# Kernel optimization log

Hardware: AMD Instinct MI355X
Metric: run time of the kernel (lower is better)

## Reference

```python
import jax, jax.numpy as jnp
import numpy as np

N_QUBITS = 21
N_LAYERS = 3

# standard CNOT (control = first wire), reshaped for tensor contraction
_CNOT = np.array([[1, 0, 0, 0],
                  [0, 1, 0, 0],
                  [0, 0, 0, 1],
                  [0, 0, 1, 0]], dtype=np.complex64).reshape(2, 2, 2, 2)


def _rot(phi, theta, omega):
    """Rot(phi, theta, omega) = RZ(omega) RY(theta) RZ(phi), 2x2 complex64."""
    c = jnp.cos(theta * 0.5)
    s = jnp.sin(theta * 0.5)
    ep = jnp.exp(-0.5j * (phi + omega))   # e^{-i(phi+omega)/2}
    em = jnp.exp(0.5j * (phi - omega))    # e^{+i(phi-omega)/2}
    row0 = jnp.stack([ep * c, -em * s])
    row1 = jnp.stack([jnp.conj(em) * s, jnp.conj(ep) * c])
    return jnp.stack([row0, row1])


def _apply_1q(U, state, q):
    # contract gate with qubit axis q of state (shape (2,)*n)
    return jnp.moveaxis(jnp.tensordot(U, state, axes=((1,), (q,))), 0, q)


def _apply_cnot(state, q):
    # CNOT on adjacent qubits (q, q+1)
    out = jnp.tensordot(jnp.asarray(_CNOT), state, axes=((2, 3), (q, q + 1)))
    return jnp.moveaxis(out, (0, 1), (q, q + 1))


def _classifier(param, feat):
    n_layers, n_qubits = param.shape[0], param.shape[1]
    state = feat.astype(jnp.complex64).reshape((2,) * n_qubits)
    for i in range(n_layers):
        # layer of single-qubit Rot gates (== kron of per-qubit 2x2 unitaries)
        for j in range(n_qubits):
            U = _rot(param[i, j, 0], param[i, j, 1], param[i, j, 2])
            state = _apply_1q(U, state, j)
        # CNOT_layer: first pairs (0,1),(2,3),... then pairs (1,2),(3,4),...
        for q in range(0, n_qubits - 1, 2):
            state = _apply_cnot(state, q)
        for q in range(1, n_qubits - 1, 2):
            state = _apply_cnot(state, q)
    # sum over even flat indices == last qubit in |0>
    amp0 = state[..., 0]
    return jnp.sum(amp0.real ** 2 + amp0.imag ** 2)


def setup_inputs() -> dict:
    key = jax.random.key(0)
    k1, k2 = jax.random.split(key)
    feat = jax.random.normal(k1, (2 ** N_QUBITS,), dtype=jnp.float32)
    param = jax.random.uniform(k2, (N_LAYERS, N_QUBITS, 3),
                               dtype=jnp.float32,
                               minval=0.0, maxval=2.0 * np.pi)
    return {"feat": feat, "param": param}


def reference(feat, param):
    return _classifier(param, feat)
```

## Files before the change

### kernel.cpp

```cpp
#include <hip/hip_runtime.h>
#include <hip/hip_fp16.h>


typedef __attribute__((ext_vector_type(2))) float f2;

union H4 { int4 i4; __half2 h[4]; };
union H2 { int2 i2; __half2 h[2]; };

__device__ __forceinline__ f2 mkf2(float a, float b) { f2 r; r.x = a; r.y = b; return r; }

__device__ __forceinline__ unsigned SWZ(unsigned i) {
    return i ^ ((i >> 4) & 0xFu) ^ ((i >> 8) & 0xFu);
}
__device__ __forceinline__ unsigned f1(unsigned x, unsigned m) {
    return x ^ ((x >> 1) & m);
}
__device__ __forceinline__ unsigned f2fold(unsigned x, unsigned mA, unsigned mB) {
    unsigned t = x ^ ((x >> 1) & mA);
    return t ^ ((t >> 1) & mB);
}

__device__ __forceinline__ void crot(const f2 u00, const f2 u01,
                                     const f2 u10, const f2 u11,
                                     f2& a, f2& b) {
    const f2 sa = mkf2(-a.y, a.x);
    const f2 sb = mkf2(-b.y, b.x);
    f2 na = u00.x * a;
    na += u00.y * sa;
    na += u01.x * b;
    na += u01.y * sb;
    f2 nb = u10.x * a;
    nb += u10.y * sa;
    nb += u11.x * b;
    nb += u11.y * sb;
    a = na; b = nb;
}

__device__ __forceinline__ void apply4(f2 v[16], const f2* gU,
                                       int id0, int id1, int id2, int id3) {
    const int ids[4] = {id0, id1, id2, id3};
#pragma unroll
    for (int kk = 0; kk < 4; ++kk) {
        const int id = ids[kk];
        if (id < 0) continue;
        const f2 u00 = gU[4*id+0], u01 = gU[4*id+1];
        const f2 u10 = gU[4*id+2], u11 = gU[4*id+3];
#pragma unroll
        for (int x = 0; x < 16; ++x)
            if (!(x & (1 << kk)))
                crot(u00, u01, u10, u11, v[x], v[x | (1 << kk)]);
    }
}

__device__ __forceinline__ void prep_gates_lds(const float* __restrict__ param,
                                               f2* gU, unsigned tid) {
    if (tid < 63) {
        float phi = param[3*tid+0], th = param[3*tid+1], om = param[3*tid+2];
        float s, c;   __sincosf(0.5f*th, &s, &c);
        float sp, cp; __sincosf(-0.5f*(phi+om), &sp, &cp);
        float sm, cm; __sincosf( 0.5f*(phi-om), &sm, &cm);
        gU[4*tid+0] = mkf2( cp*c,  sp*c);
        gU[4*tid+1] = mkf2(-cm*s, -sm*s);
        gU[4*tid+2] = mkf2( cm*s, -sm*s);
        gU[4*tid+3] = mkf2( cp*c, -sp*c);
    }
}

__device__ __forceinline__ unsigned E1A (unsigned t, unsigned r){ return (t<<4)|r; }
__device__ __forceinline__ unsigned E2A (unsigned t, unsigned r){ return ((t>>4)<<8)|(r<<4)|(t&15u); }
__device__ __forceinline__ unsigned E3A (unsigned t, unsigned r){ return ((t>>8)<<12)|(r<<8)|(t&255u); }
__device__ __forceinline__ unsigned E4A (unsigned t, unsigned r){
    return (t&127u) | (((t>>7)&3u)<<10) | ((r&1u)<<7) | (((r>>1)&1u)<<8) | (((r>>2)&1u)<<9) | (((r>>3)&1u)<<12);
}
__device__ __forceinline__ unsigned E5A (unsigned t, unsigned r){
    return (t&31u) | (((t>>5)&7u)<<7) | (((t>>8)&1u)<<12) | ((r&1u)<<5) | (((r>>1)&1u)<<6) | (((r>>2)&1u)<<10) | (((r>>3)&1u)<<11);
}
__device__ __forceinline__ unsigned E6A (unsigned t, unsigned r){ return (t&1u) | (((t>>1)&255u)<<5) | (r<<1); }
__device__ __forceinline__ unsigned E7A (unsigned t, unsigned r){
    return ((t&63u)<<1) | (((t>>6)&7u)<<10) | (r&1u) | (((r>>1)&1u)<<7) | (((r>>2)&1u)<<8) | (((r>>3)&1u)<<9);
}
__device__ __forceinline__ unsigned E8A (unsigned t, unsigned r){ return (t&7u) | (((t>>3)&63u)<<7) | ((r&15u)<<3); }
__device__ __forceinline__ unsigned E11A(unsigned t, unsigned r){
    return (r&7u) | (((r>>3)&1u)<<8) | ((t&15u)<<9) | ((t>>4)<<3);
}
__device__ __forceinline__ unsigned E1Bn(unsigned t, unsigned r){ return (t&127u) | (r<<7); }
__device__ __forceinline__ unsigned E2Bn(unsigned t, unsigned r){ return (t&7u) | (r<<3) | ((t>>3)<<7); }
__device__ __forceinline__ unsigned E5Bn(unsigned t, unsigned r){
    return (t&3u) | ((r&1u)<<2) | (((t>>2)&31u)<<3) | (((r>>1)&1u)<<8) | (((r>>2)&1u)<<9) | (((r>>3)&1u)<<10);
}
__device__ __forceinline__ unsigned E6Bn(unsigned t, unsigned r){ return (t&15u) | (r<<4) | ((t>>4)<<8); }
__device__ __forceinline__ unsigned E7Bn(unsigned t, unsigned r){ return (r&15u) | (t<<4); }

template<class FW, class FR>
__device__ __forceinline__ void phase16(f2* buf, f2 v[16], unsigned tid, FW fw, FR fr) {
    const unsigned wb = fw(tid, 0u);
#pragma unroll
    for (unsigned r = 0; r < 16; ++r) buf[wb ^ fw(0u, r)] = v[r];
    __syncthreads();
    const unsigned rb = fr(tid, 0u);
#pragma unroll
    for (unsigned r = 0; r < 16; ++r) v[r] = buf[rb ^ fr(0u, r)];
}
template<class FW, class FR>
__device__ __forceinline__ void phase16_nb(f2* buf, f2 v[16], unsigned tid, FW fw, FR fr) {
    const unsigned wb = fw(tid, 0u);
#pragma unroll
    for (unsigned r = 0; r < 16; ++r) buf[wb ^ fw(0u, r)] = v[r];
    const unsigned rb = fr(tid, 0u);
#pragma unroll
    for (unsigned r = 0; r < 16; ++r) v[r] = buf[rb ^ fr(0u, r)];
}

__global__ __launch_bounds__(512, 2) void sweepA(const float* __restrict__ feat,
                                                 const float* __restrict__ param,
                                                 __half2* __restrict__ zbuf,
                                                 float* __restrict__ out) {
    __shared__ f2 sh0[8192];
    __shared__ f2 sh1[8192];
    __shared__ f2 gU[252];
    const unsigned tid = threadIdx.x;
    const unsigned F = blockIdx.x;
    if (F == 0 && tid == 0) out[0] = 0.0f;

    float4 fraw[4];
    {
        const float4* fp = (const float4*)(feat + (((size_t)F) << 13) + (tid << 4));
#pragma unroll
        for (int c = 0; c < 4; ++c) fraw[c] = fp[c];
    }
    prep_gates_lds(param, gU, tid);

    f2 v[16];
#pragma unroll
    for (int c = 0; c < 4; ++c) {
        v[4*c+0] = mkf2(fraw[c].x, 0.f); v[4*c+1] = mkf2(fraw[c].y, 0.f);
        v[4*c+2] = mkf2(fraw[c].z, 0.f); v[4*c+3] = mkf2(fraw[c].w, 0.f);
    }
    __syncthreads();

    apply4(v, gU, 20, 19, 18, 17);
    phase16_nb(sh0, v, tid,
        [](unsigned t, unsigned r){ return SWZ(E1A(t,r)); },
        [](unsigned t, unsigned r){ return SWZ(E2A(t,r)); });
    apply4(v, gU, 16, 15, 14, 13);
    phase16(sh1, v, tid,
        [](unsigned t, unsigned r){ return SWZ(E2A(t,r)); },
        [](unsigned t, unsigned r){ return SWZ(E3A(t,r)); });
    apply4(v, gU, 12, 11, 10, 9);
    phase16(sh0, v, tid,
        [](unsigned t, unsigned r){ return SWZ(E3A(t,r)); },
        [](unsigned t, unsigned r){ return SWZ(f2fold(E4A(t,r), 0x155u, 0x2AAu)); });
    apply4(v, gU, 34, 33, 32, 8);
    phase16(sh1, v, tid,
        [](unsigned t, unsigned r){ return SWZ(E4A(t,r)); },
        [](unsigned t, unsigned r){ return SWZ(f2fold(E5A(t,r), 0x400u, 0x800u)); });
    apply4(v, gU, 36, 35, 31, 30);
    phase16(sh0, v, tid,
        [](unsigned t, unsigned r){ return SWZ(E5A(t,r)); },
        [](unsigned t, unsigned r){ return SWZ(f2fold(E6A(t,r), 0x140u, 0x2A0u)); });
    apply4(v, gU, 40, 39, 38, 37);
    phase16(sh1, v, tid,
        [](unsigned t, unsigned r){ return SWZ(E6A(t,r)); },
        [](unsigned t, unsigned r){ return SWZ(f2fold(E7A(t,r), 0x014u, 0x00Au)); });
    apply4(v, gU, 41, 55, 54, 53);
    phase16(sh0, v, tid,
        [](unsigned t, unsigned r){ return SWZ(E7A(t,r)); },
        [](unsigned t, unsigned r){ return SWZ(f1(E8A(t,r), 0x081u)); });
    apply4(v, gU, 59, 58, 57, 56);
    phase16(sh1, v, tid,
        [](unsigned t, unsigned r){ return SWZ(E8A(t,r)); },
        [](unsigned t, unsigned r){ return SWZ(f2fold(E11A(t,r), 0x050u, 0x028u)); });
    apply4(v, gU, 62, 61, 60, -1);

    {
        int2* zb2 = (int2*)zbuf;
        const unsigned sbase = (tid & 15u) | (F << 4) | ((tid >> 4) << 15);
#pragma unroll
        for (unsigned g = 0; g < 8; ++g) {
            H2 y;
            y.h[0] = __float22half2_rn(make_float2(v[g].x,      v[g].y));
            y.h[1] = __float22half2_rn(make_float2(v[g | 8u].x, v[g | 8u].y));
            zb2[sbase | (g << 12)] = y.i2;
        }
    }
}

__global__ __launch_bounds__(128, 2) void sweepB(const __half2* __restrict__ zbuf,
                                                 const float* __restrict__ param,
                                                 float* __restrict__ out) {
    __shared__ f2 sh0[2048];
    __shared__ f2 sh1[2048];
    __shared__ f2 gU[252];
    __shared__ float wsum[2];
    const unsigned tid = threadIdx.x;
    const unsigned b = ((blockIdx.x & 7u) << 6) | (blockIdx.x >> 3);
    const unsigned B8 = (b >> 2) << 1;
    const unsigned t0 = B8 ^ ((B8 >> 1) & 5u);
    const unsigned Bp8 = t0 ^ ((t0 >> 1) & 2u);
    const unsigned zbase = (b & 1u) | (((b >> 1) & 1u) << 1) | (Bp8 << 13);

    __half2 raw[16];
    {
        const __half2* zp = zbuf + zbase + (tid << 2);
#pragma unroll
        for (int r = 0; r < 16; ++r) raw[r] = zp[(size_t)r << 9];
    }
    prep_gates_lds(param, gU, tid);

    f2 v[16];
#pragma unroll
    for (int r = 0; r < 16; ++r) {
        float2 t2 = __half22float2(raw[r]);
        v[r] = mkf2(t2.x, t2.y);
    }
    __syncthreads();
    apply4(v, gU, 3, 2, 1, 0);
    phase16(sh1, v, tid,
        [](unsigned t, unsigned r){ return SWZ(E1Bn(t,r)); },
        [](unsigned t, unsigned r){ return SWZ(f1(E2Bn(t,r), 0x280u)); });
    apply4(v, gU, 7, 6, 5, 4);
    phase16(sh0, v, tid,
        [](unsigned t, unsigned r){ return SWZ(E2Bn(t,r)); },
        [](unsigned t, unsigned r){ return SWZ(f2fold(E1Bn(t,r), 0x154u, 0x028u)); });
    apply4(v, gU, 24, 23, 22, 21);
    phase16(sh1, v, tid,
        [](unsigned t, unsigned r){ return SWZ(E1Bn(t,r)); },
        [](unsigned t, unsigned r){ return SWZ(f1(E2Bn(t,r), 0x280u)); });
    apply4(v, gU, 28, 27, 26, 25);
    phase16(sh0, v, tid,
        [](unsigned t, unsigned r){ return SWZ(E2Bn(t,r)); },
        [](unsigned t, unsigned r){ return SWZ(f2fold(E5Bn(t,r), 0x150u, 0x028u)); });
    apply4(v, gU, 29, 44, 43, 42);
    phase16(sh1, v, tid,
        [](unsigned t, unsigned r){ return SWZ(E5Bn(t,r)); },
        [](unsigned t, unsigned r){ return SWZ(f2fold(E6Bn(t,r), 0x005u, 0x002u)); });
    apply4(v, gU, 48, 47, 46, 45);
    phase16_nb(sh0, v, tid,
        [](unsigned t, unsigned r){ return SWZ(E6Bn(t,r)); },
        [](unsigned t, unsigned r){ return SWZ(E7Bn(t,r)); });
    apply4(v, gU, 52, 51, 50, 49);
    float acc = 0.f;
#pragma unroll
    for (int r = 0; r < 16; ++r) acc += v[r].x*v[r].x + v[r].y*v[r].y;
    for (int off = 32; off; off >>= 1) acc += __shfl_down(acc, off);
    if ((tid & 63u) == 0) wsum[tid >> 6] = acc;
    __syncthreads();
    if (tid == 0) atomicAdd(out, wsum[0] + wsum[1]);
}

extern "C" void kernel_launch(void* const* d_in, const int* in_sizes, int n_in,
                              void* d_out, int out_size, void* d_ws, size_t ws_size,
                              hipStream_t stream) {
    const float* feat  = (const float*)d_in[0];
    const float* param = (const float*)d_in[1];
    float* out = (float*)d_out;
    __half2* zbuf = (__half2*)d_ws;

    sweepA<<<256, 512, 0, stream>>>(feat, param, zbuf, out);
    sweepB<<<512, 128, 0, stream>>>(zbuf, param, out);
}
```

Before: 43.03 us.

## Apply grouped rotation gates in sweepA via bf16 MFMA matrix products

```diff
diff --git a/kernel.cpp b/kernel.cpp
--- a/kernel.cpp
+++ b/kernel.cpp
@@ -3,11 +3,18 @@
 
 
 typedef __attribute__((ext_vector_type(2))) float f2;
-
-union H4 { int4 i4; __half2 h[4]; };
+typedef __attribute__((ext_vector_type(8))) short short8;
+typedef __attribute__((ext_vector_type(16))) float f32x16;
+
 union H2 { int2 i2; __half2 h[2]; };
 
 __device__ __forceinline__ f2 mkf2(float a, float b) { f2 r; r.x = a; r.y = b; return r; }
+
+__device__ __forceinline__ short bf16(float x) {
+    union { float f; unsigned u; } v; v.f = x;
+    unsigned u = v.u + 0x7FFFu + ((v.u >> 16) & 1u);
+    return (short)(u >> 16);
+}
 
 __device__ __forceinline__ unsigned SWZ(unsigned i) {
     return i ^ ((i >> 4) & 0xFu) ^ ((i >> 8) & 0xFu);
@@ -18,6 +25,10 @@
 __device__ __forceinline__ unsigned f2fold(unsigned x, unsigned mA, unsigned mB) {
     unsigned t = x ^ ((x >> 1) & mA);
     return t ^ ((t >> 1) & mB);
+}
+__device__ __forceinline__ unsigned ginv(unsigned y, unsigned mB, unsigned mA) {
+    unsigned t = y ^ ((y >> 1) & mB);
+    return t ^ ((t >> 1) & mA);
 }
 
 __device__ __forceinline__ void crot(const f2 u00, const f2 u01,
@@ -25,17 +36,10 @@
                                      f2& a, f2& b) {
     const f2 sa = mkf2(-a.y, a.x);
     const f2 sb = mkf2(-b.y, b.x);
-    f2 na = u00.x * a;
-    na += u00.y * sa;
-    na += u01.x * b;
-    na += u01.y * sb;
-    f2 nb = u10.x * a;
-    nb += u10.y * sa;
-    nb += u11.x * b;
-    nb += u11.y * sb;
+    f2 na = u00.x * a; na += u00.y * sa; na += u01.x * b; na += u01.y * sb;
+    f2 nb = u10.x * a; nb += u10.y * sa; nb += u11.x * b; nb += u11.y * sb;
     a = na; b = nb;
 }
-
 __device__ __forceinline__ void apply4(f2 v[16], const f2* gU,
                                        int id0, int id1, int id2, int id3) {
     const int ids[4] = {id0, id1, id2, id3};
@@ -66,23 +70,189 @@
     }
 }
 
-__device__ __forceinline__ unsigned E1A (unsigned t, unsigned r){ return (t<<4)|r; }
-__device__ __forceinline__ unsigned E2A (unsigned t, unsigned r){ return ((t>>4)<<8)|(r<<4)|(t&15u); }
-__device__ __forceinline__ unsigned E3A (unsigned t, unsigned r){ return ((t>>8)<<12)|(r<<8)|(t&255u); }
-__device__ __forceinline__ unsigned E4A (unsigned t, unsigned r){
-    return (t&127u) | (((t>>7)&3u)<<10) | ((r&1u)<<7) | (((r>>1)&1u)<<8) | (((r>>2)&1u)<<9) | (((r>>3)&1u)<<12);
-}
-__device__ __forceinline__ unsigned E5A (unsigned t, unsigned r){
-    return (t&31u) | (((t>>5)&7u)<<7) | (((t>>8)&1u)<<12) | ((r&1u)<<5) | (((r>>1)&1u)<<6) | (((r>>2)&1u)<<10) | (((r>>3)&1u)<<11);
-}
-__device__ __forceinline__ unsigned E6A (unsigned t, unsigned r){ return (t&1u) | (((t>>1)&255u)<<5) | (r<<1); }
-__device__ __forceinline__ unsigned E7A (unsigned t, unsigned r){
-    return ((t&63u)<<1) | (((t>>6)&7u)<<10) | (r&1u) | (((r>>1)&1u)<<7) | (((r>>2)&1u)<<8) | (((r>>3)&1u)<<9);
-}
-__device__ __forceinline__ unsigned E8A (unsigned t, unsigned r){ return (t&7u) | (((t>>3)&63u)<<7) | ((r&15u)<<3); }
-__device__ __forceinline__ unsigned E11A(unsigned t, unsigned r){
-    return (r&7u) | (((r>>3)&1u)<<8) | ((t&15u)<<9) | ((t>>4)<<3);
-}
+__device__ __forceinline__ unsigned E1A (unsigned n, unsigned j){ return (n<<4)|j; }
+__device__ __forceinline__ unsigned E2A (unsigned n, unsigned j){ return ((n>>4)<<8)|(j<<4)|(n&15u); }
+__device__ __forceinline__ unsigned E3A (unsigned n, unsigned j){ return ((n>>8)<<12)|(j<<8)|(n&255u); }
+__device__ __forceinline__ unsigned E4A (unsigned n, unsigned j){
+    return (n&127u) | (((n>>7)&3u)<<10) | ((j&1u)<<7) | (((j>>1)&1u)<<8) | (((j>>2)&1u)<<9) | (((j>>3)&1u)<<12);
+}
+__device__ __forceinline__ unsigned E5A (unsigned n, unsigned j){
+    return (n&31u) | (((n>>5)&7u)<<7) | (((n>>8)&1u)<<12) | ((j&1u)<<5) | (((j>>1)&1u)<<6) | (((j>>2)&1u)<<10) | (((j>>3)&1u)<<11);
+}
+__device__ __forceinline__ unsigned E6A (unsigned n, unsigned j){ return (n&1u) | (((n>>1)&255u)<<5) | (j<<1); }
+__device__ __forceinline__ unsigned E7A (unsigned n, unsigned j){
+    return ((n&63u)<<1) | (((n>>6)&7u)<<10) | (j&1u) | (((j>>1)&1u)<<7) | (((j>>2)&1u)<<8) | (((j>>3)&1u)<<9);
+}
+__device__ __forceinline__ unsigned E8A (unsigned n, unsigned j){ return (n&7u) | (((n>>3)&63u)<<7) | ((j&15u)<<3); }
+
+__device__ __forceinline__ unsigned PHS(unsigned n, unsigned j) {
+    return (n << 5) ^ ((((j >> 3) & 1u) ^ ((n >> 1) & 3u)) << 3) ^ (j & 7u);
+}
+__device__ __forceinline__ unsigned Wf2(unsigned y) {
+    unsigned n = (y&15u) | (((y>>8)&31u)<<4), j = (y>>4)&15u; return PHS(n, j);
+}
+__device__ __forceinline__ unsigned Wf3(unsigned y) {
+    unsigned n = (y&255u) | (((y>>12)&1u)<<8), j = (y>>8)&15u; return PHS(n, j);
+}
+__device__ __forceinline__ unsigned Wf4(unsigned y) {
+    unsigned x = ginv(y, 0x2AAu, 0x155u);
+    unsigned n = (x&127u) | (((x>>10)&3u)<<7);
+    unsigned j = ((x>>7)&1u) | (((x>>8)&1u)<<1) | (((x>>9)&1u)<<2) | (((x>>12)&1u)<<3);
+    return PHS(n, j);
+}
+__device__ __forceinline__ unsigned Wf5(unsigned y) {
+    unsigned x = ginv(y, 0x800u, 0x400u);
+    unsigned n = (x&31u) | (((x>>7)&7u)<<5) | (((x>>12)&1u)<<8);
+    unsigned j = ((x>>5)&1u) | (((x>>6)&1u)<<1) | (((x>>10)&1u)<<2) | (((x>>11)&1u)<<3);
+    return PHS(n, j);
+}
+__device__ __forceinline__ unsigned Wf6(unsigned y) {
+    unsigned x = ginv(y, 0x2A0u, 0x140u);
+    unsigned n = (x&1u) | (((x>>5)&255u)<<1), j = (x>>1)&15u;
+    return PHS(n, j);
+}
+__device__ __forceinline__ unsigned Wf7(unsigned y) {
+    unsigned x = ginv(y, 0x00Au, 0x014u);
+    unsigned n = ((x>>1)&63u) | (((x>>10)&7u)<<6);
+    unsigned j = (x&1u) | (((x>>7)&1u)<<1) | (((x>>8)&1u)<<2) | (((x>>9)&1u)<<3);
+    return PHS(n, j);
+}
+__device__ __forceinline__ unsigned Wf8(unsigned y) {
+    unsigned x = f1(y, 0x081u);
+    unsigned n = (x&7u) | (((x>>7)&63u)<<3), j = (x>>3)&15u;
+    return PHS(n, j);
+}
+__device__ __forceinline__ unsigned Wf9(unsigned y) {
+    unsigned x = ginv(y, 0x028u, 0x050u);
+    unsigned n = ((x>>9)&15u) | (((x>>3)&31u)<<4);
+    unsigned j = (x&7u) | (((x>>8)&1u)<<3);
+    return PHS(n, j);
+}
+
+__device__ __constant__ int GIDS[9][4] = {
+    {20,19,18,17},{16,15,14,13},{12,11,10,9},{34,33,32,8},{36,35,31,30},
+    {40,39,38,37},{41,55,54,53},{59,58,57,56},{62,61,60,-1}
+};
+
+#define MFMA_GRP(GIDX, CUR, EPREV, WNEXT) do { \
+    const short8 A1 = *(const short8*)&Ast[((GIDX)*2+0)*512 + lan*16 + h*8]; \
+    const short8 A2 = *(const short8*)&Ast[((GIDX)*2+1)*512 + lan*16 + h*8]; \
+    f32x16 ac0 = {}, ac1 = {}; \
+    { const short8 B1 = *(const short8*)&stb[CUR][(n0<<5) ^ ((h ^ ((n0>>1)&3u))<<3)]; \
+      const short8 B2 = *(const short8*)&stb[CUR][(n0<<5) ^ (((2u|h) ^ ((n0>>1)&3u))<<3)]; \
+      ac0 = __builtin_amdgcn_mfma_f32_32x32x16_bf16(A1, B1, ac0, 0, 0, 0); \
+      ac0 = __builtin_amdgcn_mfma_f32_32x32x16_bf16(A2, B2, ac0, 0, 0, 0); } \
+    { const short8 B1 = *(const short8*)&stb[CUR][(n1<<5) ^ ((h ^ ((n1>>1)&3u))<<3)]; \
+      const short8 B2 = *(const short8*)&stb[CUR][(n1<<5) ^ (((2u|h) ^ ((n1>>1)&3u))<<3)]; \
+      ac1 = __builtin_amdgcn_mfma_f32_32x32x16_bf16(A1, B1, ac1, 0, 0, 0); \
+      ac1 = __builtin_amdgcn_mfma_f32_32x32x16_bf16(A2, B2, ac1, 0, 0, 0); } \
+    const unsigned sb0 = WNEXT(EPREV(n0, jh)); \
+    const unsigned sb1 = WNEXT(EPREV(n1, jh)); \
+    _Pragma("unroll") \
+    for (unsigned p = 0; p < 16; ++p) { \
+        const unsigned sc = WNEXT(EPREV(0u, (p&3u) | (((p>>2)&1u)<<3))) ^ ((p>>3)<<4); \
+        stb[(CUR)^1][sb0 ^ sc] = bf16(ac0[p]); \
+        stb[(CUR)^1][sb1 ^ sc] = bf16(ac1[p]); \
+    } \
+    __syncthreads(); \
+} while (0)
+
+__global__ __launch_bounds__(512) void sweepA(const float* __restrict__ feat,
+                                              const float* __restrict__ param,
+                                              __half2* __restrict__ zbuf,
+                                              float* __restrict__ out) {
+    __shared__ short stb[2][16384];
+    __shared__ short Ast[9216];
+    __shared__ f2 gU[252];
+    const unsigned tid = threadIdx.x;
+    const unsigned F = blockIdx.x;
+    const unsigned wv = tid >> 6, l = tid & 63u, lan = l & 31u, h = l >> 5;
+    const unsigned n0 = wv*64u + lan, n1 = n0 + 32u;
+    const unsigned jh = h << 2;
+    if (F == 0 && tid == 0) out[0] = 0.0f;
+
+    const float4* fp0 = (const float4*)(feat + ((size_t)F << 13) + (n0 << 4) + (h << 3));
+    const float4* fp1 = (const float4*)(feat + ((size_t)F << 13) + (n1 << 4) + (h << 3));
+    float4 fa0 = fp0[0], fb0 = fp0[1], fa1 = fp1[0], fb1 = fp1[1];
+
+    prep_gates_lds(param, gU, tid);
+    __syncthreads();
+
+    for (unsigned ent = tid; ent < 9216u; ent += 512u) {
+        const unsigned g = ent >> 10, rem = ent & 1023u;
+        const unsigned a12 = rem >> 9, m = (rem >> 4) & 31u, k = rem & 15u;
+        const unsigned i = m & 15u, ihi = m >> 4;
+        float wr = 1.f, wi = 0.f;
+#pragma unroll
+        for (int kk = 0; kk < 4; ++kk) {
+            const int id = GIDS[g][kk];
+            const unsigned ib = (i >> kk) & 1u, kb = (k >> kk) & 1u;
+            if (id < 0) { if (ib != kb) { wr = 0.f; wi = 0.f; } }
+            else {
+                const f2 u = gU[4*id + (ib<<1) + kb];
+                const float nr = wr*u.x - wi*u.y, ni = wr*u.y + wi*u.x;
+                wr = nr; wi = ni;
+            }
+        }
+        const float val = (a12 == 0) ? (ihi ? wi : wr) : (ihi ? wr : -wi);
+        Ast[ent] = bf16(val);
+    }
+    __syncthreads();
+
+    {
+        const short8 A1 = *(const short8*)&Ast[0*512 + lan*16 + h*8];
+        f32x16 ac0 = {}, ac1 = {};
+        const short8 B0 = { bf16(fa0.x), bf16(fa0.y), bf16(fa0.z), bf16(fa0.w),
+                            bf16(fb0.x), bf16(fb0.y), bf16(fb0.z), bf16(fb0.w) };
+        const short8 Bb = { bf16(fa1.x), bf16(fa1.y), bf16(fa1.z), bf16(fa1.w),
+                            bf16(fb1.x), bf16(fb1.y), bf16(fb1.z), bf16(fb1.w) };
+        ac0 = __builtin_amdgcn_mfma_f32_32x32x16_bf16(A1, B0, ac0, 0, 0, 0);
+        ac1 = __builtin_amdgcn_mfma_f32_32x32x16_bf16(A1, Bb, ac1, 0, 0, 0);
+        const unsigned sb0 = Wf2(E1A(n0, jh));
+        const unsigned sb1 = Wf2(E1A(n1, jh));
+#pragma unroll
+        for (unsigned p = 0; p < 16; ++p) {
+            const unsigned sc = Wf2(E1A(0u, (p&3u) | (((p>>2)&1u)<<3))) ^ ((p>>3)<<4);
+            stb[0][sb0 ^ sc] = bf16(ac0[p]);
+            stb[0][sb1 ^ sc] = bf16(ac1[p]);
+        }
+        __syncthreads();
+    }
+    MFMA_GRP(1, 0, E2A, Wf3);
+    MFMA_GRP(2, 1, E3A, Wf4);
+    MFMA_GRP(3, 0, E4A, Wf5);
+    MFMA_GRP(4, 1, E5A, Wf6);
+    MFMA_GRP(5, 0, E6A, Wf7);
+    MFMA_GRP(6, 1, E7A, Wf8);
+    MFMA_GRP(7, 0, E8A, Wf9);
+    {
+        const short8 A1 = *(const short8*)&Ast[(8*2+0)*512 + lan*16 + h*8];
+        const short8 A2 = *(const short8*)&Ast[(8*2+1)*512 + lan*16 + h*8];
+        f32x16 ac0 = {}, ac1 = {};
+        { const short8 B1 = *(const short8*)&stb[1][(n0<<5) ^ ((h ^ ((n0>>1)&3u))<<3)];
+          const short8 B2 = *(const short8*)&stb[1][(n0<<5) ^ (((2u|h) ^ ((n0>>1)&3u))<<3)];
+          ac0 = __builtin_amdgcn_mfma_f32_32x32x16_bf16(A1, B1, ac0, 0, 0, 0);
+          ac0 = __builtin_amdgcn_mfma_f32_32x32x16_bf16(A2, B2, ac0, 0, 0, 0); }
+        { const short8 B1 = *(const short8*)&stb[1][(n1<<5) ^ ((h ^ ((n1>>1)&3u))<<3)];
+          const short8 B2 = *(const short8*)&stb[1][(n1<<5) ^ (((2u|h) ^ ((n1>>1)&3u))<<3)];
+          ac1 = __builtin_amdgcn_mfma_f32_32x32x16_bf16(A1, B1, ac1, 0, 0, 0);
+          ac1 = __builtin_amdgcn_mfma_f32_32x32x16_bf16(A2, B2, ac1, 0, 0, 0); }
+        int2* zb2 = (int2*)zbuf;
+        const unsigned base = (lan & 15u) | (F << 4) | (((lan >> 4) & 1u) << 15);
+#pragma unroll
+        for (unsigned p = 0; p < 4; ++p) {
+            const unsigned jf = ((p & 3u) | (h << 2)) << 12;
+            H2 y0, y1;
+            y0.h[0] = __float22half2_rn(make_float2(ac0[p],      ac0[p+8]));
+            y0.h[1] = __float22half2_rn(make_float2(ac0[p+4],    ac0[p+12]));
+            y1.h[0] = __float22half2_rn(make_float2(ac1[p],      ac1[p+8]));
+            y1.h[1] = __float22half2_rn(make_float2(ac1[p+4],    ac1[p+12]));
+            zb2[base | jf | ((n0 >> 5) << 16)] = y0.i2;
+            zb2[base | jf | ((n1 >> 5) << 16)] = y1.i2;
+        }
+    }
+}
+
 __device__ __forceinline__ unsigned E1Bn(unsigned t, unsigned r){ return (t&127u) | (r<<7); }
 __device__ __forceinline__ unsigned E2Bn(unsigned t, unsigned r){ return (t&7u) | (r<<3) | ((t>>3)<<7); }
 __device__ __forceinline__ unsigned E5Bn(unsigned t, unsigned r){
@@ -109,80 +279,6 @@
     const unsigned rb = fr(tid, 0u);
 #pragma unroll
     for (unsigned r = 0; r < 16; ++r) v[r] = buf[rb ^ fr(0u, r)];
-}
-
-__global__ __launch_bounds__(512, 2) void sweepA(const float* __restrict__ feat,
-                                                 const float* __restrict__ param,
-                                                 __half2* __restrict__ zbuf,
-                                                 float* __restrict__ out) {
-    __shared__ f2 sh0[8192];
-    __shared__ f2 sh1[8192];
-    __shared__ f2 gU[252];
-    const unsigned tid = threadIdx.x;
-    const unsigned F = blockIdx.x;
-    if (F == 0 && tid == 0) out[0] = 0.0f;
-
-    float4 fraw[4];
-    {
-        const float4* fp = (const float4*)(feat + (((size_t)F) << 13) + (tid << 4));
-#pragma unroll
-        for (int c = 0; c < 4; ++c) fraw[c] = fp[c];
-    }
-    prep_gates_lds(param, gU, tid);
-
-    f2 v[16];
-#pragma unroll
-    for (int c = 0; c < 4; ++c) {
-        v[4*c+0] = mkf2(fraw[c].x, 0.f); v[4*c+1] = mkf2(fraw[c].y, 0.f);
-        v[4*c+2] = mkf2(fraw[c].z, 0.f); v[4*c+3] = mkf2(fraw[c].w, 0.f);
-    }
-    __syncthreads();
-
-    apply4(v, gU, 20, 19, 18, 17);
-    phase16_nb(sh0, v, tid,
-        [](unsigned t, unsigned r){ return SWZ(E1A(t,r)); },
-        [](unsigned t, unsigned r){ return SWZ(E2A(t,r)); });
-    apply4(v, gU, 16, 15, 14, 13);
-    phase16(sh1, v, tid,
-        [](unsigned t, unsigned r){ return SWZ(E2A(t,r)); },
-        [](unsigned t, unsigned r){ return SWZ(E3A(t,r)); });
-    apply4(v, gU, 12, 11, 10, 9);
-    phase16(sh0, v, tid,
-        [](unsigned t, unsigned r){ return SWZ(E3A(t,r)); },
-        [](unsigned t, unsigned r){ return SWZ(f2fold(E4A(t,r), 0x155u, 0x2AAu)); });
-    apply4(v, gU, 34, 33, 32, 8);
-    phase16(sh1, v, tid,
-        [](unsigned t, unsigned r){ return SWZ(E4A(t,r)); },
-        [](unsigned t, unsigned r){ return SWZ(f2fold(E5A(t,r), 0x400u, 0x800u)); });
-    apply4(v, gU, 36, 35, 31, 30);
-    phase16(sh0, v, tid,
-        [](unsigned t, unsigned r){ return SWZ(E5A(t,r)); },
-        [](unsigned t, unsigned r){ return SWZ(f2fold(E6A(t,r), 0x140u, 0x2A0u)); });
-    apply4(v, gU, 40, 39, 38, 37);
-    phase16(sh1, v, tid,
-        [](unsigned t, unsigned r){ return SWZ(E6A(t,r)); },
-        [](unsigned t, unsigned r){ return SWZ(f2fold(E7A(t,r), 0x014u, 0x00Au)); });
-    apply4(v, gU, 41, 55, 54, 53);
-    phase16(sh0, v, tid,
-        [](unsigned t, unsigned r){ return SWZ(E7A(t,r)); },
-        [](unsigned t, unsigned r){ return SWZ(f1(E8A(t,r), 0x081u)); });
-    apply4(v, gU, 59, 58, 57, 56);
-    phase16(sh1, v, tid,
-        [](unsigned t, unsigned r){ return SWZ(E8A(t,r)); },
-        [](unsigned t, unsigned r){ return SWZ(f2fold(E11A(t,r), 0x050u, 0x028u)); });
-    apply4(v, gU, 62, 61, 60, -1);
-
-    {
-        int2* zb2 = (int2*)zbuf;
-        const unsigned sbase = (tid & 15u) | (F << 4) | ((tid >> 4) << 15);
-#pragma unroll
-        for (unsigned g = 0; g < 8; ++g) {
-            H2 y;
-            y.h[0] = __float22half2_rn(make_float2(v[g].x,      v[g].y));
-            y.h[1] = __float22half2_rn(make_float2(v[g | 8u].x, v[g | 8u].y));
-            zb2[sbase | (g << 12)] = y.i2;
-        }
-    }
 }
 
 __global__ __launch_bounds__(128, 2) void sweepB(const __half2* __restrict__ zbuf,
```

Result: no change. 43.03 us (-0.0%).
